# Optimization experiments

Measured on AMD Instinct MI355X. Metric: run time of the kernel, lower is better.

## Reference

```python
import jax, jax.numpy as jnp
import numpy as np

B, N, X, Y, W1, W2 = 1, 6, 16, 16, 8, 8
DIM, HEADS, DH = 128, 4, 32
INNER = HEADS * DH
EPS = 1e-5


def setup_inputs() -> dict:
    key = jax.random.key(0)
    ks = jax.random.split(key, 8)
    s = 0.02
    shp = (B, N, X, Y, W1, W2, DIM)
    return {
        "q": jax.random.normal(ks[0], shp, jnp.float32),
        "k": jax.random.normal(ks[1], shp, jnp.float32),
        "v": jax.random.normal(ks[2], shp, jnp.float32),
        "ln_q_g": jnp.ones((DIM,), jnp.float32), "ln_q_b": jnp.zeros((DIM,), jnp.float32),
        "ln_k_g": jnp.ones((DIM,), jnp.float32), "ln_k_b": jnp.zeros((DIM,), jnp.float32),
        "ln_v_g": jnp.ones((DIM,), jnp.float32), "ln_v_b": jnp.zeros((DIM,), jnp.float32),
        "Wq": jax.random.normal(ks[3], (DIM, INNER), jnp.float32) * s, "bq": jnp.zeros((INNER,), jnp.float32),
        "Wk": jax.random.normal(ks[4], (DIM, INNER), jnp.float32) * s, "bk": jnp.zeros((INNER,), jnp.float32),
        "Wv": jax.random.normal(ks[5], (DIM, INNER), jnp.float32) * s, "bv": jnp.zeros((INNER,), jnp.float32),
        "Wp": jax.random.normal(ks[6], (INNER, DIM), jnp.float32) * s, "bp": jnp.zeros((DIM,), jnp.float32),
    }


def _layernorm(x, g, b):
    m = x.mean(-1, keepdims=True)
    v = x.var(-1, keepdims=True)
    return (x - m) / jnp.sqrt(v + EPS) * g + b


def _to_windows(t):
    # 'b n x y w1 w2 d -> b (x y) (n w1 w2) d'
    b, n, x, y, w1, w2, d = t.shape
    t = jnp.transpose(t, (0, 2, 3, 1, 4, 5, 6))
    return t.reshape(b, x * y, n * w1 * w2, d)


def _norm_proj_heads(t, g, bb, W, bias):
    # norm + linear, then 'b l t (h d) -> b h l t d'
    t = _layernorm(t, g, bb) @ W + bias
    b, L, T, _ = t.shape
    t = t.reshape(b, L, T, HEADS, DH)
    return jnp.transpose(t, (0, 3, 1, 2, 4))


def reference(q, k, v, ln_q_g, ln_q_b, ln_k_g, ln_k_b, ln_v_g, ln_v_b,
              Wq, bq, Wk, bk, Wv, bv, Wp, bp):
    qh = _norm_proj_heads(_to_windows(q), ln_q_g, ln_q_b, Wq, bq)  # (b,h,L,Q,dh)
    kh = _norm_proj_heads(_to_windows(k), ln_k_g, ln_k_b, Wk, bk)
    vh = _norm_proj_heads(_to_windows(v), ln_v_g, ln_v_b, Wv, bv)
    scale = DH ** -0.5
    dot = scale * jnp.einsum('bhlqd,bhlkd->bhlqk', qh, kh)  # (b,h,L,Q,K)
    att = jax.nn.softmax(dot, axis=-1)
    a = jnp.einsum('bhlqk,bhlkd->bhlqd', att, vh)  # (b,h,L,Q,dh)
    # merge heads: 'b h l q d -> b l q (h d)'
    a = jnp.transpose(a, (0, 2, 3, 1, 4)).reshape(B, X * Y, N * W1 * W2, INNER)
    z = a @ Wp + bp  # (b, L, Q, DIM)
    # 'b (x y) (n w1 w2) d -> b n x y w1 w2 d' then mean over n
    z = z.reshape(B, X, Y, N, W1, W2, DIM)
    z = jnp.transpose(z, (0, 3, 1, 2, 4, 5, 6)).mean(axis=1)
    return z  # (b, x, y, w1, w2, DIM)
```

## Files before the change

kernel.cpp:

```cpp
#include <hip/hip_runtime.h>
#include <hip/hip_bf16.h>

typedef unsigned short u16;
typedef __attribute__((ext_vector_type(8))) short b16x8;
typedef __attribute__((ext_vector_type(4))) float f32x4;

__device__ __forceinline__ u16 f2bf(float f) {
    union { float f; unsigned int u; } v; v.f = f;
    unsigned int u = v.u;
    return (u16)((u + 0x7FFFu + ((u >> 16) & 1u)) >> 16);
}

__global__ __launch_bounds__(256) void k_pack_w(const float* __restrict__ w0,
                                                const float* __restrict__ w1,
                                                const float* __restrict__ w2,
                                                const float* __restrict__ w3,
                                                u16* __restrict__ dstbase) {
    const int b = blockIdx.x;
    const int tensor = b >> 2;
    const float* src = (tensor == 0) ? w0 : (tensor == 1) ? w1
                     : (tensor == 2) ? w2 : w3;
    u16* dst = dstbase + tensor * 16384;
    const int i0 = (b & 3) * 4096;
    for (int j = threadIdx.x; j < 4096; j += 256) {
        int i = i0 + j;
        int k = i >> 7, n = i & 127;
        int kc = k >> 3, kr = k & 7;
        dst[n * 128 + ((kc ^ (n & 7)) << 3) + kr] = f2bf(src[i]);
    }
}

struct K1Args {
    const float* x[3];
    const float* lng[3];
    const float* lnb[3];
    const float* bias[3];
    u16* outQ; u16* outK; u16* outVt;
};

__global__ __launch_bounds__(512, 4) void k_ln_proj(K1Args a, const u16* __restrict__ wt) {
    __shared__ u16 sW[16384];
    __shared__ u16 sA[16384];
    const int tid = threadIdx.x;
    const int tensor = blockIdx.y;
    const int wv = tid >> 6;

    const u16* wsrc = wt + tensor * 16384;
#pragma unroll
    for (int it = 0; it < 4; ++it) {
        int e = (it * 512 + tid) << 3;
        *(b16x8*)(sW + e) = *(const b16x8*)(wsrc + e);
    }

    const int r = tid >> 2, sub = tid & 3;
    const int token0 = blockIdx.x * 128;
    const int l = token0 / 384;
    const int tloc0 = token0 % 384;
    const int ti = tloc0 + r;
    const int nn = ti >> 6, w = ti & 63;
    const float* rowp = a.x[tensor] + (size_t)(nn * 16384 + l * 64 + w) * 128 + sub * 32;
    float v[32];
    float s = 0.f, s2 = 0.f;
#pragma unroll
    for (int j = 0; j < 32; j += 4) {
        float4 f = *(const float4*)(rowp + j);
        v[j] = f.x; v[j + 1] = f.y; v[j + 2] = f.z; v[j + 3] = f.w;
        s  += (f.x + f.y) + (f.z + f.w);
        s2 += (f.x * f.x + f.y * f.y) + (f.z * f.z + f.w * f.w);
    }
    s  += __shfl_xor(s, 1);  s  += __shfl_xor(s, 2);
    s2 += __shfl_xor(s2, 1); s2 += __shfl_xor(s2, 2);
    const float mean = s * (1.f / 128.f);
    const float rstd = rsqrtf(s2 * (1.f / 128.f) - mean * mean + 1e-5f);
    const float* gp = a.lng[tensor];
    const float* bbp = a.lnb[tensor];
#pragma unroll
    for (int j = 0; j < 32; j += 8) {
        int k0 = sub * 32 + j;
        b16x8 tv;
#pragma unroll
        for (int q = 0; q < 8; ++q) {
            int k = k0 + q;
            tv[q] = (short)f2bf((v[j + q] - mean) * rstd * gp[k] + bbp[k]);
        }
        *(b16x8*)(sA + r * 128 + (((k0 >> 3) ^ (r & 7)) << 3)) = tv;
    }
    __syncthreads();

    const int lane = tid & 63, lr = lane & 15, lg = lane >> 4;
    f32x4 acc[8];
#pragma unroll
    for (int i = 0; i < 8; ++i) acc[i] = (f32x4){0.f, 0.f, 0.f, 0.f};
    const int rowA = wv * 16 + lr;
#pragma unroll
    for (int kt = 0; kt < 4; ++kt) {
        const int ch = kt * 4 + lg;
        b16x8 af = *(const b16x8*)(sA + rowA * 128 + ((ch ^ (rowA & 7)) << 3));
#pragma unroll
        for (int nt = 0; nt < 8; ++nt) {
            const int nc = nt * 16 + lr;
            b16x8 bf = *(const b16x8*)(sW + nc * 128 + ((ch ^ (nc & 7)) << 3));
            acc[nt] = __builtin_amdgcn_mfma_f32_16x16x32_bf16(af, bf, acc[nt], 0, 0, 0);
        }
    }

    const float* biasp = a.bias[tensor];
    if (tensor != 2) {
        const float scale = (tensor == 0) ? 0.17677669529663687f : 1.0f;
        u16* outp = (tensor == 0) ? a.outQ : a.outK;
#pragma unroll
        for (int nt = 0; nt < 8; ++nt) {
            const int col = nt * 16 + lr;
            const float bb = biasp[col];
#pragma unroll
            for (int rg = 0; rg < 4; ++rg) {
                const int rowl = wv * 16 + lg * 4 + rg;
                float val = (acc[nt][rg] + bb) * scale;
                int cch = col >> 3;
                sA[rowl * 128 + ((cch ^ (rowl & 7)) << 3) + (col & 7)] = f2bf(val);
            }
        }
        const int rrow = wv * 16 + (lane >> 2);
#pragma unroll
        for (int c = 0; c < 4; ++c) {
            int colc = (lane & 3) + c * 4;
            b16x8 val = *(const b16x8*)(sA + rrow * 128 + ((colc ^ (rrow & 7)) << 3));
            *(b16x8*)(outp + (size_t)(token0 + rrow) * 128 + colc * 8) = val;
        }
    } else {
        __syncthreads();
#pragma unroll
        for (int nt = 0; nt < 8; ++nt) {
            const int col = nt * 16 + lr;
            const float bb = biasp[col];
#pragma unroll
            for (int rg = 0; rg < 4; ++rg) {
                const int trowl = wv * 16 + lg * 4 + rg;
                float val = acc[nt][rg] + bb;
                int tch = trowl >> 3;
                sA[col * 128 + ((tch ^ (col & 7)) << 3) + (trowl & 7)] = f2bf(val);
            }
        }
        __syncthreads();
        const int f = tid >> 2;
        const size_t vb = ((size_t)(l * 4 + (f >> 5)) * 32 + (f & 31)) * 384 + tloc0;
#pragma unroll
        for (int c = 0; c < 4; ++c) {
            int tch = (tid & 3) + c * 4;
            b16x8 val = *(const b16x8*)(sA + f * 128 + ((tch ^ (f & 7)) << 3));
            *(b16x8*)(a.outVt + vb + tch * 8) = val;
        }
    }
}

__global__ __launch_bounds__(256, 3) void k_attn(const u16* __restrict__ qh,
                                                 const u16* __restrict__ kh,
                                                 const u16* __restrict__ vt,
                                                 u16* __restrict__ ah) {
    __shared__ u16 sK[384 * 32];
    __shared__ u16 sP[4][16 * 104];
    const int tid = threadIdx.x;
    const int l = blockIdx.x, h = blockIdx.y;
    const size_t baseQ = ((size_t)l * 384) * 128 + h * 32;
    const size_t baseV = ((size_t)(l * 4 + h) * 32) * 384;

#pragma unroll
    for (int it = 0; it < 6; ++it) {
        int idx = it * 256 + tid;
        int t = idx >> 2, c = idx & 3;
        b16x8 kv = *(const b16x8*)(kh + baseQ + (size_t)t * 128 + c * 8);
        *(b16x8*)(sK + t * 32 + ((c ^ (t & 3)) << 3)) = kv;
    }
    __syncthreads();

    const int wv = tid >> 6, lane = tid & 63, lr = lane & 15, lg = lane >> 4;
    u16* myP = sP[wv];

    for (int qt = wv; qt < 24; qt += 4) {
        b16x8 qf = *(const b16x8*)(qh + baseQ + (size_t)(qt * 16 + lr) * 128 + lg * 8);
        f32x4 sacc[24];
#pragma unroll
        for (int kt = 0; kt < 24; ++kt) {
            const int t = kt * 16 + lr;
            b16x8 kf = *(const b16x8*)(sK + t * 32 + ((lg ^ (t & 3)) << 3));
            sacc[kt] = __builtin_amdgcn_mfma_f32_16x16x32_bf16(
                qf, kf, (f32x4){0.f, 0.f, 0.f, 0.f}, 0, 0, 0);
        }
        float sm[4];
#pragma unroll
        for (int rg = 0; rg < 4; ++rg) {
            float m = sacc[0][rg];
#pragma unroll
            for (int kt = 1; kt < 24; ++kt) m = fmaxf(m, sacc[kt][rg]);
            m = fmaxf(m, __shfl_xor(m, 1));
            m = fmaxf(m, __shfl_xor(m, 2));
            m = fmaxf(m, __shfl_xor(m, 4));
            m = fmaxf(m, __shfl_xor(m, 8));
            float ss = 0.f;
#pragma unroll
            for (int kt = 0; kt < 24; ++kt) {
                float e = __expf(sacc[kt][rg] - m);
                sacc[kt][rg] = e;
                ss += e;
            }
            ss += __shfl_xor(ss, 1); ss += __shfl_xor(ss, 2);
            ss += __shfl_xor(ss, 4); ss += __shfl_xor(ss, 8);
            sm[rg] = ss;
        }
        f32x4 pacc[2];
        pacc[0] = (f32x4){0.f, 0.f, 0.f, 0.f};
        pacc[1] = (f32x4){0.f, 0.f, 0.f, 0.f};
#pragma unroll
        for (int chunk = 0; chunk < 4; ++chunk) {
#pragma unroll
            for (int kc = 0; kc < 6; ++kc) {
                const int kt = chunk * 6 + kc;
#pragma unroll
                for (int rg = 0; rg < 4; ++rg) {
                    int q = lg * 4 + rg;
                    int tl = kc * 16 + lr;
                    myP[q * 104 + tl] = f2bf(sacc[kt][rg]);
                }
            }
#pragma unroll
            for (int k2 = 0; k2 < 3; ++k2) {
                b16x8 pf = *(const b16x8*)(myP + lr * 104 + k2 * 32 + lg * 8);
#pragma unroll
                for (int nt = 0; nt < 2; ++nt) {
                    b16x8 vf = *(const b16x8*)(vt + baseV +
                                               (size_t)(nt * 16 + lr) * 384 +
                                               chunk * 96 + k2 * 32 + lg * 8);
                    pacc[nt] = __builtin_amdgcn_mfma_f32_16x16x32_bf16(pf, vf, pacc[nt], 0, 0, 0);
                }
            }
        }
#pragma unroll
        for (int nt = 0; nt < 2; ++nt) {
#pragma unroll
            for (int rg = 0; rg < 4; ++rg) {
                float aa = pacc[nt][rg] / sm[rg];
                size_t trow = (size_t)(qt * 16 + lg * 4 + rg);
                ah[baseQ + trow * 128 + nt * 16 + lr] = f2bf(aa);
            }
        }
    }
}

__global__ __launch_bounds__(512, 2) void k_proj_mean(const u16* __restrict__ ah,
                                                      const u16* __restrict__ wtp,
                                                      const float* __restrict__ bp,
                                                      float* __restrict__ out) {
    __shared__ u16 sW[16384];
    const int tid = threadIdx.x;
    const int l = blockIdx.x;
#pragma unroll
    for (int it = 0; it < 4; ++it) {
        int e = (it * 512 + tid) << 3;
        *(b16x8*)(sW + e) = *(const b16x8*)(wtp + e);
    }
    __syncthreads();
    const int wv8 = tid >> 6;
    const int wm = wv8 >> 1, wn = wv8 & 1;
    const int lane = tid & 63, lr = lane & 15, lg = lane >> 4;
    f32x4 acc[4];
#pragma unroll
    for (int i = 0; i < 4; ++i) acc[i] = (f32x4){0.f, 0.f, 0.f, 0.f};
#pragma unroll
    for (int nn = 0; nn < 6; ++nn) {
        const int mt = wm + nn * 4;
        const size_t rowb = ((size_t)l * 384 + mt * 16 + lr) * 128;
#pragma unroll
        for (int kt = 0; kt < 4; ++kt) {
            b16x8 af = *(const b16x8*)(ah + rowb + kt * 32 + lg * 8);
            const int ch = kt * 4 + lg;
#pragma unroll
            for (int nt = 0; nt < 4; ++nt) {
                const int nc = (wn * 4 + nt) * 16 + lr;
                b16x8 bf = *(const b16x8*)(sW + nc * 128 + ((ch ^ (nc & 7)) << 3));
                acc[nt] = __builtin_amdgcn_mfma_f32_16x16x32_bf16(af, bf, acc[nt], 0, 0, 0);
            }
        }
    }
#pragma unroll
    for (int nt = 0; nt < 4; ++nt) {
        const int col = (wn * 4 + nt) * 16 + lr;
        const float bb = bp[col];
#pragma unroll
        for (int rg = 0; rg < 4; ++rg) {
            const int wrow = wm * 16 + lg * 4 + rg;
            out[((size_t)l * 64 + wrow) * 128 + col] = acc[nt][rg] * (1.0f / 6.0f) + bb;
        }
    }
}

extern "C" void kernel_launch(void* const* d_in, const int* in_sizes, int n_in,
                              void* d_out, int out_size, void* d_ws, size_t ws_size,
                              hipStream_t stream) {
    (void)in_sizes; (void)n_in; (void)out_size; (void)ws_size;
    const float* q      = (const float*)d_in[0];
    const float* k      = (const float*)d_in[1];
    const float* v      = (const float*)d_in[2];
    const float* ln_q_g = (const float*)d_in[3];
    const float* ln_q_b = (const float*)d_in[4];
    const float* ln_k_g = (const float*)d_in[5];
    const float* ln_k_b = (const float*)d_in[6];
    const float* ln_v_g = (const float*)d_in[7];
    const float* ln_v_b = (const float*)d_in[8];
    const float* Wq     = (const float*)d_in[9];
    const float* bq     = (const float*)d_in[10];
    const float* Wk     = (const float*)d_in[11];
    const float* bk     = (const float*)d_in[12];
    const float* Wv     = (const float*)d_in[13];
    const float* bv     = (const float*)d_in[14];
    const float* Wp     = (const float*)d_in[15];
    const float* bp     = (const float*)d_in[16];
    float* out = (float*)d_out;

    u16* ws = (u16*)d_ws;
    const long long MATE = 98304LL * 128;
    u16* wQ  = ws;
    u16* wK  = ws + MATE;
    u16* wVt = ws + 2 * MATE;
    u16* wA  = ws + 3 * MATE;
    u16* wWt = ws + 4 * MATE;

    k_pack_w<<<16, 256, 0, stream>>>(Wq, Wk, Wv, Wp, wWt);

    K1Args args;
    args.x[0] = q;       args.x[1] = k;       args.x[2] = v;
    args.lng[0] = ln_q_g; args.lng[1] = ln_k_g; args.lng[2] = ln_v_g;
    args.lnb[0] = ln_q_b; args.lnb[1] = ln_k_b; args.lnb[2] = ln_v_b;
    args.bias[0] = bq;   args.bias[1] = bk;   args.bias[2] = bv;
    args.outQ = wQ;      args.outK = wK;      args.outVt = wVt;
    k_ln_proj<<<dim3(768, 3), 512, 0, stream>>>(args, wWt);

    k_attn<<<dim3(256, 4), 256, 0, stream>>>(wQ, wK, wVt, wA);

    k_proj_mean<<<256, 512, 0, stream>>>(wA, wWt + 3 * 16384, bp, out);
}
```

Measured before the change: 349.9 us.

## Head-major Q/K/A layout, online softmax in attention, split projection grid

Q, K and attention output are now stored head-major (l,h,token,dh), so each attention block reads contiguous K and Q tiles. Attention switches to a two-pass online softmax that uses exp2 with log2e folded into the Q scale, keeping fewer score registers live, and drops the occupancy hint. The LN-projection kernel reads weights straight from global memory instead of staging them in LDS, and the output projection is split over four column blocks with a smaller LDS tile. Several unrelated changes land together, including bf16 conversion through the HIP intrinsic and an extra K swizzle term.

```diff
diff --git a/kernel.cpp b/kernel.cpp
--- a/kernel.cpp
+++ b/kernel.cpp
@@ -6,9 +6,9 @@
 typedef __attribute__((ext_vector_type(4))) float f32x4;
 
 __device__ __forceinline__ u16 f2bf(float f) {
-    union { float f; unsigned int u; } v; v.f = f;
-    unsigned int u = v.u;
-    return (u16)((u + 0x7FFFu + ((u >> 16) & 1u)) >> 16);
+    union { __hip_bfloat16 h; u16 u; } c;
+    c.h = __float2bfloat16(f);
+    return c.u;
 }
 
 __global__ __launch_bounds__(256) void k_pack_w(const float* __restrict__ w0,
@@ -39,18 +39,11 @@
 };
 
 __global__ __launch_bounds__(512, 4) void k_ln_proj(K1Args a, const u16* __restrict__ wt) {
-    __shared__ u16 sW[16384];
     __shared__ u16 sA[16384];
     const int tid = threadIdx.x;
     const int tensor = blockIdx.y;
     const int wv = tid >> 6;
-
     const u16* wsrc = wt + tensor * 16384;
-#pragma unroll
-    for (int it = 0; it < 4; ++it) {
-        int e = (it * 512 + tid) << 3;
-        *(b16x8*)(sW + e) = *(const b16x8*)(wsrc + e);
-    }
 
     const int r = tid >> 2, sub = tid & 3;
     const int token0 = blockIdx.x * 128;
@@ -85,7 +78,6 @@
         }
         *(b16x8*)(sA + r * 128 + (((k0 >> 3) ^ (r & 7)) << 3)) = tv;
     }
-    __syncthreads();
 
     const int lane = tid & 63, lr = lane & 15, lg = lane >> 4;
     f32x4 acc[8];
@@ -99,14 +91,16 @@
 #pragma unroll
         for (int nt = 0; nt < 8; ++nt) {
             const int nc = nt * 16 + lr;
-            b16x8 bf = *(const b16x8*)(sW + nc * 128 + ((ch ^ (nc & 7)) << 3));
+            b16x8 bf = *(const b16x8*)(wsrc + nc * 128 + ((ch ^ (nc & 7)) << 3));
             acc[nt] = __builtin_amdgcn_mfma_f32_16x16x32_bf16(af, bf, acc[nt], 0, 0, 0);
         }
     }
 
     const float* biasp = a.bias[tensor];
     if (tensor != 2) {
-        const float scale = (tensor == 0) ? 0.17677669529663687f : 1.0f;
+        const float scale = (tensor == 0)
+            ? 0.17677669529663687f * 1.4426950408889634f
+            : 1.0f;
         u16* outp = (tensor == 0) ? a.outQ : a.outK;
 #pragma unroll
         for (int nt = 0; nt < 8; ++nt) {
@@ -116,8 +110,7 @@
             for (int rg = 0; rg < 4; ++rg) {
                 const int rowl = wv * 16 + lg * 4 + rg;
                 float val = (acc[nt][rg] + bb) * scale;
-                int cch = col >> 3;
-                sA[rowl * 128 + ((cch ^ (rowl & 7)) << 3) + (col & 7)] = f2bf(val);
+                sA[rowl * 128 + (((col >> 3) ^ (rowl & 7)) << 3) + (col & 7)] = f2bf(val);
             }
         }
         const int rrow = wv * 16 + (lane >> 2);
@@ -125,7 +118,8 @@
         for (int c = 0; c < 4; ++c) {
             int colc = (lane & 3) + c * 4;
             b16x8 val = *(const b16x8*)(sA + rrow * 128 + ((colc ^ (rrow & 7)) << 3));
-            *(b16x8*)(outp + (size_t)(token0 + rrow) * 128 + colc * 8) = val;
+            int head = colc >> 2, dh0 = (colc & 3) * 8;
+            *(b16x8*)(outp + ((size_t)(l * 4 + head) * 384 + tloc0 + rrow) * 32 + dh0) = val;
         }
     } else {
         __syncthreads();
@@ -137,8 +131,7 @@
             for (int rg = 0; rg < 4; ++rg) {
                 const int trowl = wv * 16 + lg * 4 + rg;
                 float val = acc[nt][rg] + bb;
-                int tch = trowl >> 3;
-                sA[col * 128 + ((tch ^ (col & 7)) << 3) + (trowl & 7)] = f2bf(val);
+                sA[col * 128 + (((trowl >> 3) ^ (col & 7)) << 3) + (trowl & 7)] = f2bf(val);
             }
         }
         __syncthreads();
@@ -153,23 +146,23 @@
     }
 }
 
-__global__ __launch_bounds__(256, 3) void k_attn(const u16* __restrict__ qh,
-                                                 const u16* __restrict__ kh,
-                                                 const u16* __restrict__ vt,
-                                                 u16* __restrict__ ah) {
+__global__ __launch_bounds__(256) void k_attn(const u16* __restrict__ qh,
+                                              const u16* __restrict__ kh,
+                                              const u16* __restrict__ vt,
+                                              u16* __restrict__ ah) {
     __shared__ u16 sK[384 * 32];
     __shared__ u16 sP[4][16 * 104];
     const int tid = threadIdx.x;
     const int l = blockIdx.x, h = blockIdx.y;
-    const size_t baseQ = ((size_t)l * 384) * 128 + h * 32;
-    const size_t baseV = ((size_t)(l * 4 + h) * 32) * 384;
+    const size_t base = (size_t)(l * 4 + h) * 12288;
 
 #pragma unroll
     for (int it = 0; it < 6; ++it) {
         int idx = it * 256 + tid;
         int t = idx >> 2, c = idx & 3;
-        b16x8 kv = *(const b16x8*)(kh + baseQ + (size_t)t * 128 + c * 8);
-        *(b16x8*)(sK + t * 32 + ((c ^ (t & 3)) << 3)) = kv;
+        b16x8 kv = *(const b16x8*)(kh + base + (size_t)idx * 8);
+        int sw = (c ^ (t & 3) ^ ((t >> 2) & 3)) & 3;
+        *(b16x8*)(sK + t * 32 + (sw << 3)) = kv;
     }
     __syncthreads();
 
@@ -177,113 +170,128 @@
     u16* myP = sP[wv];
 
     for (int qt = wv; qt < 24; qt += 4) {
-        b16x8 qf = *(const b16x8*)(qh + baseQ + (size_t)(qt * 16 + lr) * 128 + lg * 8);
-        f32x4 sacc[24];
-#pragma unroll
-        for (int kt = 0; kt < 24; ++kt) {
-            const int t = kt * 16 + lr;
-            b16x8 kf = *(const b16x8*)(sK + t * 32 + ((lg ^ (t & 3)) << 3));
-            sacc[kt] = __builtin_amdgcn_mfma_f32_16x16x32_bf16(
-                qf, kf, (f32x4){0.f, 0.f, 0.f, 0.f}, 0, 0, 0);
-        }
-        float sm[4];
-#pragma unroll
-        for (int rg = 0; rg < 4; ++rg) {
-            float m = sacc[0][rg];
-#pragma unroll
-            for (int kt = 1; kt < 24; ++kt) m = fmaxf(m, sacc[kt][rg]);
-            m = fmaxf(m, __shfl_xor(m, 1));
-            m = fmaxf(m, __shfl_xor(m, 2));
-            m = fmaxf(m, __shfl_xor(m, 4));
-            m = fmaxf(m, __shfl_xor(m, 8));
-            float ss = 0.f;
-#pragma unroll
-            for (int kt = 0; kt < 24; ++kt) {
-                float e = __expf(sacc[kt][rg] - m);
-                sacc[kt][rg] = e;
-                ss += e;
-            }
-            ss += __shfl_xor(ss, 1); ss += __shfl_xor(ss, 2);
-            ss += __shfl_xor(ss, 4); ss += __shfl_xor(ss, 8);
-            sm[rg] = ss;
-        }
+        b16x8 qf = *(const b16x8*)(qh + base + (size_t)(qt * 16 + lr) * 32 + lg * 8);
+        float mrun[4] = {-1e30f, -1e30f, -1e30f, -1e30f};
+        float srun[4] = {0.f, 0.f, 0.f, 0.f};
         f32x4 pacc[2];
         pacc[0] = (f32x4){0.f, 0.f, 0.f, 0.f};
         pacc[1] = (f32x4){0.f, 0.f, 0.f, 0.f};
 #pragma unroll
-        for (int chunk = 0; chunk < 4; ++chunk) {
-#pragma unroll
-            for (int kc = 0; kc < 6; ++kc) {
-                const int kt = chunk * 6 + kc;
-#pragma unroll
-                for (int rg = 0; rg < 4; ++rg) {
-                    int q = lg * 4 + rg;
-                    int tl = kc * 16 + lr;
-                    myP[q * 104 + tl] = f2bf(sacc[kt][rg]);
+        for (int half = 0; half < 2; ++half) {
+            f32x4 sacc[12];
+#pragma unroll
+            for (int kt = 0; kt < 12; ++kt) {
+                const int t = half * 192 + kt * 16 + lr;
+                const int sw = (lg ^ (t & 3) ^ ((t >> 2) & 3)) & 3;
+                b16x8 kf = *(const b16x8*)(sK + t * 32 + (sw << 3));
+                sacc[kt] = __builtin_amdgcn_mfma_f32_16x16x32_bf16(
+                    qf, kf, (f32x4){0.f, 0.f, 0.f, 0.f}, 0, 0, 0);
+            }
+#pragma unroll
+            for (int rg = 0; rg < 4; ++rg) {
+                float m6[6];
+#pragma unroll
+                for (int i = 0; i < 6; ++i)
+                    m6[i] = fmaxf(sacc[2 * i][rg], sacc[2 * i + 1][rg]);
+                float tm = fmaxf(fmaxf(fmaxf(m6[0], m6[1]), fmaxf(m6[2], m6[3])),
+                                 fmaxf(m6[4], m6[5]));
+                tm = fmaxf(tm, __shfl_xor(tm, 1));
+                tm = fmaxf(tm, __shfl_xor(tm, 2));
+                tm = fmaxf(tm, __shfl_xor(tm, 4));
+                tm = fmaxf(tm, __shfl_xor(tm, 8));
+                const float mnew = fmaxf(mrun[rg], tm);
+                const float corr = exp2f(mrun[rg] - mnew);
+                pacc[0][rg] *= corr;
+                pacc[1][rg] *= corr;
+                float s6[6];
+#pragma unroll
+                for (int i = 0; i < 6; ++i) {
+                    float e0 = exp2f(sacc[2 * i][rg] - mnew);
+                    float e1 = exp2f(sacc[2 * i + 1][rg] - mnew);
+                    sacc[2 * i][rg] = e0; sacc[2 * i + 1][rg] = e1;
+                    s6[i] = e0 + e1;
                 }
-            }
-#pragma unroll
-            for (int k2 = 0; k2 < 3; ++k2) {
-                b16x8 pf = *(const b16x8*)(myP + lr * 104 + k2 * 32 + lg * 8);
-#pragma unroll
-                for (int nt = 0; nt < 2; ++nt) {
-                    b16x8 vf = *(const b16x8*)(vt + baseV +
-                                               (size_t)(nt * 16 + lr) * 384 +
-                                               chunk * 96 + k2 * 32 + lg * 8);
-                    pacc[nt] = __builtin_amdgcn_mfma_f32_16x16x32_bf16(pf, vf, pacc[nt], 0, 0, 0);
+                srun[rg] = srun[rg] * corr +
+                           (((s6[0] + s6[1]) + (s6[2] + s6[3])) + (s6[4] + s6[5]));
+                mrun[rg] = mnew;
+            }
+#pragma unroll
+            for (int c2 = 0; c2 < 2; ++c2) {
+#pragma unroll
+                for (int kc = 0; kc < 6; ++kc) {
+#pragma unroll
+                    for (int rg = 0; rg < 4; ++rg) {
+                        int q = lg * 4 + rg;
+                        myP[q * 104 + kc * 16 + lr] = f2bf(sacc[c2 * 6 + kc][rg]);
+                    }
                 }
-            }
+#pragma unroll
+                for (int k2 = 0; k2 < 3; ++k2) {
+                    b16x8 pf = *(const b16x8*)(myP + lr * 104 + k2 * 32 + lg * 8);
+#pragma unroll
+                    for (int nt = 0; nt < 2; ++nt) {
+                        b16x8 vf = *(const b16x8*)(vt + base +
+                                                   (size_t)(nt * 16 + lr) * 384 +
+                                                   half * 192 + c2 * 96 + k2 * 32 + lg * 8);
+                        pacc[nt] = __builtin_amdgcn_mfma_f32_16x16x32_bf16(pf, vf, pacc[nt], 0, 0, 0);
+                    }
+                }
+            }
+        }
+        float rs[4];
+#pragma unroll
+        for (int rg = 0; rg < 4; ++rg) {
+            float ss = srun[rg];
+            ss += __shfl_xor(ss, 1); ss += __shfl_xor(ss, 2);
+            ss += __shfl_xor(ss, 4); ss += __shfl_xor(ss, 8);
+            rs[rg] = __builtin_amdgcn_rcpf(ss);
         }
 #pragma unroll
         for (int nt = 0; nt < 2; ++nt) {
 #pragma unroll
             for (int rg = 0; rg < 4; ++rg) {
-                float aa = pacc[nt][rg] / sm[rg];
                 size_t trow = (size_t)(qt * 16 + lg * 4 + rg);
-                ah[baseQ + trow * 128 + nt * 16 + lr] = f2bf(aa);
-            }
-        }
-    }
-}
-
-__global__ __launch_bounds__(512, 2) void k_proj_mean(const u16* __restrict__ ah,
+                ah[base + trow * 32 + nt * 16 + lr] = f2bf(pacc[nt][rg] * rs[rg]);
+            }
+        }
+    }
+}
+
+__global__ __launch_bounds__(256, 4) void k_proj_mean(const u16* __restrict__ ah,
                                                       const u16* __restrict__ wtp,
                                                       const float* __restrict__ bp,
                                                       float* __restrict__ out) {
-    __shared__ u16 sW[16384];
+    __shared__ u16 sW[4096];
     const int tid = threadIdx.x;
-    const int l = blockIdx.x;
-#pragma unroll
-    for (int it = 0; it < 4; ++it) {
-        int e = (it * 512 + tid) << 3;
-        *(b16x8*)(sW + e) = *(const b16x8*)(wtp + e);
+    const int l = blockIdx.x, cq = blockIdx.y;
+#pragma unroll
+    for (int it = 0; it < 2; ++it) {
+        int e = (it * 256 + tid) << 3;
+        *(b16x8*)(sW + e) = *(const b16x8*)(wtp + cq * 4096 + e);
     }
     __syncthreads();
-    const int wv8 = tid >> 6;
-    const int wm = wv8 >> 1, wn = wv8 & 1;
-    const int lane = tid & 63, lr = lane & 15, lg = lane >> 4;
-    f32x4 acc[4];
-#pragma unroll
-    for (int i = 0; i < 4; ++i) acc[i] = (f32x4){0.f, 0.f, 0.f, 0.f};
+    const int wm = tid >> 6, lane = tid & 63, lr = lane & 15, lg = lane >> 4;
+    f32x4 acc[2];
+    acc[0] = (f32x4){0.f, 0.f, 0.f, 0.f};
+    acc[1] = (f32x4){0.f, 0.f, 0.f, 0.f};
 #pragma unroll
     for (int nn = 0; nn < 6; ++nn) {
-        const int mt = wm + nn * 4;
-        const size_t rowb = ((size_t)l * 384 + mt * 16 + lr) * 128;
+        const int t = nn * 64 + wm * 16 + lr;
 #pragma unroll
         for (int kt = 0; kt < 4; ++kt) {
-            b16x8 af = *(const b16x8*)(ah + rowb + kt * 32 + lg * 8);
+            b16x8 af = *(const b16x8*)(ah + ((size_t)(l * 4 + kt) * 384 + t) * 32 + lg * 8);
             const int ch = kt * 4 + lg;
 #pragma unroll
-            for (int nt = 0; nt < 4; ++nt) {
-                const int nc = (wn * 4 + nt) * 16 + lr;
-                b16x8 bf = *(const b16x8*)(sW + nc * 128 + ((ch ^ (nc & 7)) << 3));
+            for (int nt = 0; nt < 2; ++nt) {
+                const int ncl = nt * 16 + lr;
+                b16x8 bf = *(const b16x8*)(sW + ncl * 128 + ((ch ^ (ncl & 7)) << 3));
                 acc[nt] = __builtin_amdgcn_mfma_f32_16x16x32_bf16(af, bf, acc[nt], 0, 0, 0);
             }
         }
     }
 #pragma unroll
-    for (int nt = 0; nt < 4; ++nt) {
-        const int col = (wn * 4 + nt) * 16 + lr;
+    for (int nt = 0; nt < 2; ++nt) {
+        const int col = cq * 32 + nt * 16 + lr;
         const float bb = bp[col];
 #pragma unroll
         for (int rg = 0; rg < 4; ++rg) {
@@ -336,5 +344,5 @@
 
     k_attn<<<dim3(256, 4), 256, 0, stream>>>(wQ, wK, wVt, wA);
 
-    k_proj_mean<<<256, 512, 0, stream>>>(wA, wWt + 3 * 16384, bp, out);
-}
+    k_proj_mean<<<dim3(256, 4), 256, 0, stream>>>(wA, wWt + 3 * 16384, bp, out);
+}
```

Measured after the change: 357.9 us. +2.3%, slower.
